# Kernel tuning notes

Measured on AMD Instinct MI355X. Metric: run time of the kernel, lower is better.

Reference implementation:

```python
import jax, jax.numpy as jnp
import numpy as np

BETA = 1.0
DEPTH = 10
LEVELS = DEPTH - 1          # decision levels along any root->leaf path
NUM_LEAVES = 2 ** LEVELS    # 512
NUM_INTERNAL = NUM_LEAVES - 1  # 511, heap-ordered: root=0, children 2i+1/2i+2


def _tree_paths():
    """For each leaf, the heap indices of its ancestors and the branch taken (0=left,1=right)."""
    anc = np.zeros((NUM_LEAVES, LEVELS), dtype=np.int32)
    bits = np.zeros((NUM_LEAVES, LEVELS), dtype=np.int32)
    for j in range(NUM_LEAVES):
        node = 0
        for t in range(LEVELS):
            bit = (j >> (LEVELS - 1 - t)) & 1
            anc[j, t] = node
            bits[j, t] = bit
            node = 2 * node + 1 + bit
    return jnp.asarray(anc), jnp.asarray(bits)

_ANC, _BITS = _tree_paths()


def setup_inputs() -> dict:
    key = jax.random.key(0)
    k1, k2, k3, k4 = jax.random.split(key, 4)
    B, F, K = 8192, 4096, 1000
    return {
        "xs": jax.random.normal(k1, (B, F), dtype=jnp.float32),
        "W": jax.random.normal(k2, (NUM_INTERNAL, F), dtype=jnp.float32) * (1.0 / np.sqrt(F)),
        "b": jax.random.normal(k3, (NUM_INTERNAL,), dtype=jnp.float32) * 0.01,
        "leaf_params": jax.random.normal(k4, (NUM_LEAVES, K), dtype=jnp.float32),
    }


def reference(xs, W, b, leaf_params):
    # All node projections as one GEMM: [B, NUM_INTERNAL]
    ps = jax.nn.sigmoid(BETA * (xs @ W.T + b))
    # Gather per-leaf ancestor probs: [B, NUM_LEAVES, LEVELS]
    g = ps[:, _ANC]
    edge = jnp.where(_BITS[None] == 1, g, 1.0 - g)
    leaf_prob = jnp.prod(edge, axis=-1)          # [B, NUM_LEAVES]
    dists = jax.nn.softmax(leaf_params, axis=-1)  # [NUM_LEAVES, K]
    return leaf_prob @ dists                      # [B, K]
```

## Files before the change

### kernel.cpp

```cpp
#include <hip/hip_runtime.h>


typedef __bf16 bf16x8 __attribute__((ext_vector_type(8)));
typedef float f32x4 __attribute__((ext_vector_type(4)));
typedef _Float16 f16x8 __attribute__((ext_vector_type(8)));

#define B_DIM 8192
#define F_DIM 4096
#define NI 511
#define NL 512
#define K_DIM 1000
#define KPAD 1024
#define SPLIT 2
#define KCHUNK 2048
#define NT_G1 32

#define W_BLKS  1024
#define SM_BLKS 512

__device__ inline unsigned short f2bf(float f) {
    unsigned int u = __float_as_uint(f);
    return (unsigned short)((u + 0x7FFFu + ((u >> 16) & 1u)) >> 16);
}
__device__ inline unsigned int pk_bf16(float a, float b) {
    return (unsigned int)f2bf(a) | ((unsigned int)f2bf(b) << 16);
}
__device__ inline unsigned int pk2_hu(float a, float b) {
    unsigned int ua = __float_as_uint(a) + 0x8000u;
    unsigned int ub = __float_as_uint(b) + 0x8000u;
    return __builtin_amdgcn_perm(ub, ua, 0x07060302u);
}

typedef __attribute__((address_space(1))) const unsigned int guint;
typedef __attribute__((address_space(3))) unsigned int luint;
__device__ inline void gload16(const unsigned short* g, unsigned short* l) {
    __builtin_amdgcn_global_load_lds((guint*)g, (luint*)l, 16, 0, 0);
}

__device__ inline bf16x8 ldb(const unsigned short* Lbase, int r, int kb) {
    const int g = (kb >> 3) ^ (r & 7);
    return *(const bf16x8*)&Lbase[r * 64 + g * 8];
}

__device__ inline float waveMax(float v) {
#pragma unroll
    for (int off = 32; off; off >>= 1) v = fmaxf(v, __shfl_down(v, off, 64));
    return v;
}
__device__ inline float waveSum(float v) {
#pragma unroll
    for (int off = 32; off; off >>= 1) v += __shfl_down(v, off, 64);
    return v;
}

__global__ __launch_bounds__(256) void prep_kernel(
    const float* __restrict__ W, unsigned short* __restrict__ Wb,
    const float* __restrict__ lp, unsigned short* __restrict__ dT)
{
    __shared__ float sred[8];
    const int bid = blockIdx.x;
    const int tid = threadIdx.x;

    if (bid < W_BLKS) {
        const size_t i = ((size_t)bid * 256 + tid) * 8;
        const int row = (int)(i >> 12);
        uint4 h = {0u, 0u, 0u, 0u};
        if (row < NI) {
            const float4 a = *(const float4*)(W + i);
            const float4 b = *(const float4*)(W + i + 4);
            h.x = pk_bf16(a.x, a.y);
            h.y = pk_bf16(a.z, a.w);
            h.z = pk_bf16(b.x, b.y);
            h.w = pk_bf16(b.z, b.w);
        }
        *(uint4*)(Wb + i) = h;
        return;
    }
    const int k = bid - W_BLKS;
    const int lane = tid & 63;
    const int wave = tid >> 6;
    const float* rowp = lp + (size_t)k * K_DIM;

    float vals[4];
    float mx = -3.0e38f;
#pragma unroll
    for (int c = 0; c < 4; ++c) {
        const int n = tid + c * 256;
        vals[c] = (n < K_DIM) ? rowp[n] : -3.0e38f;
        mx = fmaxf(mx, vals[c]);
    }
    mx = waveMax(mx);
    if (lane == 0) sred[wave] = mx;
    __syncthreads();
    const float gmax = fmaxf(fmaxf(sred[0], sred[1]), fmaxf(sred[2], sred[3]));

    float sum = 0.f;
#pragma unroll
    for (int c = 0; c < 4; ++c) {
        const int n = tid + c * 256;
        const float e = (n < K_DIM) ? __expf(vals[c] - gmax) : 0.f;
        vals[c] = e;
        sum += e;
    }
    sum = waveSum(sum);
    if (lane == 0) sred[4 + wave] = sum;
    __syncthreads();
    const float inv = 1.0f / (sred[4] + sred[5] + sred[6] + sred[7]);
#pragma unroll
    for (int c = 0; c < 4; ++c) {
        const int n = tid + c * 256;
        if (n < K_DIM) dT[(size_t)n * NL + k] = f2bf(vals[c] * inv);
    }
}

__global__ __launch_bounds__(256, 2) void gemm1_kernel(
    const float* __restrict__ A, const unsigned short* __restrict__ Bb,
    _Float16* __restrict__ part)
{
    __shared__ __align__(16) unsigned short Al[128 * 64];
    __shared__ __align__(16) unsigned short Bl[4][128 * 64];

    const int id = blockIdx.x;
    const int xcd = id & 7;
    const int j = id >> 3;
    const int nt = j & 3;
    const int z = (j >> 2) & 1;
    const int mhi = j >> 3;
    const int m0 = (mhi * 8 + xcd) * 128;
    const int n0 = nt * 128;
    const int kbeg = z * KCHUNK;

    const int tid = threadIdx.x;
    const int lane = tid & 63;
    const int wave = tid >> 6;
    const int wm = (wave >> 1) * 64;
    const int wn = (wave & 1) * 64;
    const int quad = lane >> 4;
    const int l16 = lane & 15;

    const int rowA = wave * 4 + (lane >> 4);
    const int q = lane & 15;
    const float* gA = A + (size_t)(m0 + rowA) * F_DIM + kbeg + q * 4;

    const int drb = lane >> 3;
    const int cb = ((lane & 7) ^ drb) * 8;
    const unsigned short* gB = Bb + (size_t)(n0 + wave * 8 + drb) * F_DIM + kbeg + cb;
    const int lBoff = wave * 8 * 64;

    const f32x4 zero = {0.f, 0.f, 0.f, 0.f};
    f32x4 acc[4][4];
#pragma unroll
    for (int i = 0; i < 4; ++i)
#pragma unroll
        for (int j2 = 0; j2 < 4; ++j2) acc[i][j2] = zero;

    f32x4 ab[2][8];
#pragma unroll
    for (int p = 0; p < 4; ++p)
        gload16(gB + (size_t)p * 32 * F_DIM, &Bl[0][lBoff + p * 2048]);
#pragma unroll
    for (int p = 0; p < 4; ++p)
        gload16(gB + 64 + (size_t)p * 32 * F_DIM, &Bl[1][lBoff + p * 2048]);
    __builtin_amdgcn_sched_barrier(0);
#pragma unroll
    for (int p = 0; p < 8; ++p)
        ab[0][p] = *(const f32x4*)(gA + (size_t)p * 16 * F_DIM);
#pragma unroll
    for (int p = 0; p < 8; ++p)
        ab[1][p] = *(const f32x4*)(gA + 64 + (size_t)p * 16 * F_DIM);
    __builtin_amdgcn_sched_barrier(0);

#define G1_ITER(T, DO_ISSUE, WCNT)                                             \
    {                                                                          \
        _Pragma("unroll") for (int p = 0; p < 8; ++p) {                        \
            const int r = rowA + p * 16;                                       \
            uint2 w;                                                           \
            w.x = pk2_hu(ab[(T) & 1][p].x, ab[(T) & 1][p].y);                  \
            w.y = pk2_hu(ab[(T) & 1][p].z, ab[(T) & 1][p].w);                  \
            *(uint2*)&Al[r * 64 + (((q >> 1) ^ (r & 7)) * 8) + (q & 1) * 4] = w;\
        }                                                                      \
        asm volatile("s_waitcnt vmcnt(" #WCNT ") lgkmcnt(0)" ::: "memory");    \
        __builtin_amdgcn_sched_barrier(0);                                     \
        __builtin_amdgcn_s_barrier();                                          \
        __builtin_amdgcn_sched_barrier(0);                                     \
        if (DO_ISSUE) {                                                        \
            _Pragma("unroll") for (int p = 0; p < 4; ++p)                      \
                gload16(gB + (size_t)((T) + 2) * 64 + (size_t)p * 32 * F_DIM,  \
                        &Bl[((T) + 2) & 3][lBoff + p * 2048]);                 \
            __builtin_amdgcn_sched_barrier(0);                                 \
            _Pragma("unroll") for (int p = 0; p < 8; ++p)                      \
                ab[(T) & 1][p] = *(const f32x4*)(gA + (size_t)((T) + 2) * 64   \
                                                 + (size_t)p * 16 * F_DIM);    \
        }                                                                      \
        _Pragma("unroll") for (int kk = 0; kk < 64; kk += 32) {                \
            const int kb = kk + quad * 8;                                      \
            bf16x8 av[4], bv[4];                                               \
            _Pragma("unroll") for (int i = 0; i < 4; ++i)                      \
                av[i] = ldb(Al, wm + i * 16 + l16, kb);                        \
            _Pragma("unroll") for (int j2 = 0; j2 < 4; ++j2)                   \
                bv[j2] = ldb(&Bl[(T) & 3][0], wn + j2 * 16 + l16, kb);         \
            _Pragma("unroll") for (int i = 0; i < 4; ++i)                      \
                _Pragma("unroll") for (int j2 = 0; j2 < 4; ++j2)               \
                    acc[i][j2] = __builtin_amdgcn_mfma_f32_16x16x32_bf16(      \
                        av[i], bv[j2], acc[i][j2], 0, 0, 0);                   \
        }                                                                      \
        __builtin_amdgcn_sched_barrier(0);                                     \
        __builtin_amdgcn_s_barrier();                                          \
        __builtin_amdgcn_sched_barrier(0);                                     \
    }

#pragma unroll 4
    for (int t = 0; t < NT_G1 - 4; ++t) G1_ITER(t, 1, 12);
    G1_ITER(28, 1, 12);
    G1_ITER(29, 1, 12);
    G1_ITER(30, 0, 12);
    G1_ITER(31, 0, 0);
#undef G1_ITER

    _Float16* dst = part + (size_t)z * ((size_t)B_DIM * NL);
#pragma unroll
    for (int i = 0; i < 4; ++i) {
        const int mbase = m0 + wm + i * 16 + quad * 4;
#pragma unroll
        for (int j2 = 0; j2 < 4; ++j2) {
            const int n = n0 + wn + j2 * 16 + l16;
#pragma unroll
            for (int r = 0; r < 4; ++r)
                dst[(size_t)(mbase + r) * NL + n] = (_Float16)acc[i][j2][r];
        }
    }
}

__global__ __launch_bounds__(256) void reduce_tree_kernel(
    const _Float16* __restrict__ part, const float* __restrict__ bvec,
    unsigned short* __restrict__ leafbf)
{
    __shared__ float bsh[NL];
    __shared__ float prow[4][NL];

    const int tid = threadIdx.x;
    bsh[tid] = (tid < NI) ? bvec[tid] : 0.0f;
    const int t2 = tid + 256;
    bsh[t2] = (t2 < NI) ? bvec[t2] : 0.0f;

    const int wave = tid >> 6;
    const int lane = tid & 63;
    const int row = blockIdx.x * 4 + wave;
    const size_t base = (size_t)row * NL + lane * 8;

    float v[8] = {0.f, 0.f, 0.f, 0.f, 0.f, 0.f, 0.f, 0.f};
#pragma unroll
    for (int s = 0; s < SPLIT; ++s) {
        const f16x8 h = *(const f16x8*)(part + (size_t)s * ((size_t)B_DIM * NL) + base);
#pragma unroll
        for (int e = 0; e < 8; ++e) v[e] += (float)h[e];
    }
    __syncthreads();

#pragma unroll
    for (int i = 0; i < 8; ++i) {
        const float x = v[i] + bsh[lane * 8 + i];
        prow[wave][lane * 8 + i] = 1.0f / (1.0f + __expf(-x));
    }
    __syncthreads();

    const float* pr = prow[wave];
    float pre = 1.0f;
    int pnode = 0;
#pragma unroll
    for (int t = 5; t >= 0; --t) {
        const int bit = (lane >> t) & 1;
        const float p = pr[pnode];
        pre *= bit ? p : (1.0f - p);
        pnode = 2 * pnode + 1 + bit;
    }
    unsigned short outs[8];
#pragma unroll
    for (int jj = 0; jj < 8; ++jj) {
        float prob = pre;
        int node = pnode;
#pragma unroll
        for (int t = 2; t >= 0; --t) {
            const int bit = (jj >> t) & 1;
            const float p = pr[node];
            prob *= bit ? p : (1.0f - p);
            node = 2 * node + 1 + bit;
        }
        outs[jj] = f2bf(prob);
    }
    uint4 r;
    r.x = (unsigned int)outs[0] | ((unsigned int)outs[1] << 16);
    r.y = (unsigned int)outs[2] | ((unsigned int)outs[3] << 16);
    r.z = (unsigned int)outs[4] | ((unsigned int)outs[5] << 16);
    r.w = (unsigned int)outs[6] | ((unsigned int)outs[7] << 16);
    *(uint4*)(leafbf + (size_t)row * NL + lane * 8) = r;
}

__global__ __launch_bounds__(256) void gemm2_kernel(
    const unsigned short* __restrict__ A, const unsigned short* __restrict__ Bm,
    float* __restrict__ out)
{
    __shared__ __align__(16) unsigned short Al[128 * 64];
    __shared__ __align__(16) unsigned short Bl[128 * 64];

    const int id = blockIdx.x;
    const int xcd = id & 7;
    const int j = id >> 3;
    const int nt = j & 7;
    const int mhi = j >> 3;
    const int m0 = (mhi * 8 + xcd) * 128;
    const int n0 = nt * 128;

    const int tid = threadIdx.x;
    const int lane = tid & 63;
    const int wave = tid >> 6;
    const int wm = (wave >> 1) * 64;
    const int wn = (wave & 1) * 64;
    const int quad = lane >> 4;
    const int l16 = lane & 15;

    const int drb = lane >> 3;
    const int cb = ((lane & 7) ^ drb) * 8;
    const unsigned short* gA = A + (size_t)(m0 + wave * 8 + drb) * NL + cb;
    const unsigned short* gB = Bm + (size_t)(n0 + wave * 8 + drb) * NL + cb;
    unsigned short* lA = &Al[wave * 8 * 64];
    unsigned short* lB = &Bl[wave * 8 * 64];

    const f32x4 zero = {0.f, 0.f, 0.f, 0.f};
    f32x4 acc[4][4];
#pragma unroll
    for (int i = 0; i < 4; ++i)
#pragma unroll
        for (int j2 = 0; j2 < 4; ++j2) acc[i][j2] = zero;

    for (int k0 = 0; k0 < NL; k0 += 64) {
#pragma unroll
        for (int p = 0; p < 4; ++p) {
            gload16(gA + k0 + (size_t)p * 32 * NL, lA + p * 2048);
            gload16(gB + k0 + (size_t)p * 32 * NL, lB + p * 2048);
        }
        __syncthreads();
#pragma unroll
        for (int kk = 0; kk < 64; kk += 32) {
            const int kb = kk + quad * 8;
            bf16x8 av[4], bv[4];
#pragma unroll
            for (int i = 0; i < 4; ++i)
                av[i] = ldb(Al, wm + i * 16 + l16, kb);
#pragma unroll
            for (int j2 = 0; j2 < 4; ++j2)
                bv[j2] = ldb(Bl, wn + j2 * 16 + l16, kb);
#pragma unroll
            for (int i = 0; i < 4; ++i)
#pragma unroll
                for (int j2 = 0; j2 < 4; ++j2)
                    acc[i][j2] = __builtin_amdgcn_mfma_f32_16x16x32_bf16(av[i], bv[j2], acc[i][j2], 0, 0, 0);
        }
        __syncthreads();
    }

#pragma unroll
    for (int i = 0; i < 4; ++i) {
        const int mbase = m0 + wm + i * 16 + quad * 4;
#pragma unroll
        for (int j2 = 0; j2 < 4; ++j2) {
            const int n = n0 + wn + j2 * 16 + l16;
            if (n < K_DIM) {
#pragma unroll
                for (int r = 0; r < 4; ++r)
                    out[(size_t)(mbase + r) * K_DIM + n] = acc[i][j2][r];
            }
        }
    }
}

extern "C" void kernel_launch(void* const* d_in, const int* in_sizes, int n_in,
                              void* d_out, int out_size, void* d_ws, size_t ws_size,
                              hipStream_t stream) {
    const float* xs = (const float*)d_in[0];
    const float* W  = (const float*)d_in[1];
    const float* b  = (const float*)d_in[2];
    const float* lp = (const float*)d_in[3];
    float* out = (float*)d_out;

    const size_t partB = (size_t)B_DIM * NL * 2;
    const size_t leafB = (size_t)B_DIM * NL * 2;
    const size_t dTB   = (size_t)KPAD * NL * 2;

    char* ws = (char*)d_ws;
    _Float16* part = (_Float16*)ws;
    unsigned short* leafbf = (unsigned short*)(ws + SPLIT * partB);
    unsigned short* dT = (unsigned short*)(ws + SPLIT * partB + leafB);
    unsigned short* Wb = (unsigned short*)(ws + SPLIT * partB + leafB + dTB);
    (void)ws_size;

    hipLaunchKernelGGL(prep_kernel, dim3(W_BLKS + SM_BLKS), dim3(256), 0, stream,
                       W, Wb, lp, dT);
    hipLaunchKernelGGL(gemm1_kernel, dim3(8 * 8 * 2 * 4), dim3(256), 0, stream,
                       xs, Wb, part);
    hipLaunchKernelGGL(reduce_tree_kernel, dim3(B_DIM / 4), dim3(256), 0, stream,
                       part, b, leafbf);
    hipLaunchKernelGGL(gemm2_kernel, dim3(8 * 8 * 8), dim3(256), 0, stream,
                       leafbf, dT, out);
}
```

Baseline: 263.7 us.

## Split gemm1 K three ways for higher occupancy; double-buffer gemm2 LDS loads

gemm1 now splits K into three chunks instead of two, so it launches 768 blocks instead of 512. To fit three blocks per CU it shrinks the B LDS ring from four stages to two. gemm2 gains a double-buffered LDS pipeline, so loads for the next K-slab overlap the MFMA work on the current one, replacing the old load-then-sync loop. This trades more fp16 partial-sum traffic and extra reduction work, plus a shallower prefetch in gemm1, for better occupancy and wave balance.

```diff
diff --git a/kernel.cpp b/kernel.cpp
--- a/kernel.cpp
+++ b/kernel.cpp
@@ -11,9 +11,7 @@
 #define NL 512
 #define K_DIM 1000
 #define KPAD 1024
-#define SPLIT 2
-#define KCHUNK 2048
-#define NT_G1 32
+#define SPLIT 3
 
 #define W_BLKS  1024
 #define SM_BLKS 512
@@ -113,22 +111,24 @@
     }
 }
 
-__global__ __launch_bounds__(256, 2) void gemm1_kernel(
+__global__ __launch_bounds__(256, 3) void gemm1_kernel(
     const float* __restrict__ A, const unsigned short* __restrict__ Bb,
     _Float16* __restrict__ part)
 {
     __shared__ __align__(16) unsigned short Al[128 * 64];
-    __shared__ __align__(16) unsigned short Bl[4][128 * 64];
+    __shared__ __align__(16) unsigned short Bl[2][128 * 64];
 
     const int id = blockIdx.x;
     const int xcd = id & 7;
     const int j = id >> 3;
     const int nt = j & 3;
-    const int z = (j >> 2) & 1;
-    const int mhi = j >> 3;
+    const int rem = j >> 2;
+    const int mhi = rem / 3;
+    const int z = rem - mhi * 3;
     const int m0 = (mhi * 8 + xcd) * 128;
     const int n0 = nt * 128;
-    const int kbeg = z * KCHUNK;
+    const int kbeg = z * 1408;
+    const int NT = (z == 2) ? 20 : 22;
 
     const int tid = threadIdx.x;
     const int lane = tid & 63;
@@ -158,9 +158,6 @@
 #pragma unroll
     for (int p = 0; p < 4; ++p)
         gload16(gB + (size_t)p * 32 * F_DIM, &Bl[0][lBoff + p * 2048]);
-#pragma unroll
-    for (int p = 0; p < 4; ++p)
-        gload16(gB + 64 + (size_t)p * 32 * F_DIM, &Bl[1][lBoff + p * 2048]);
     __builtin_amdgcn_sched_barrier(0);
 #pragma unroll
     for (int p = 0; p < 8; ++p)
@@ -170,27 +167,34 @@
         ab[1][p] = *(const f32x4*)(gA + 64 + (size_t)p * 16 * F_DIM);
     __builtin_amdgcn_sched_barrier(0);
 
-#define G1_ITER(T, DO_ISSUE, WCNT)                                             \
+#define G1_ITER(TVAL, PAR)                                                     \
     {                                                                          \
+        const int t_ = (TVAL);                                                 \
         _Pragma("unroll") for (int p = 0; p < 8; ++p) {                        \
             const int r = rowA + p * 16;                                       \
             uint2 w;                                                           \
-            w.x = pk2_hu(ab[(T) & 1][p].x, ab[(T) & 1][p].y);                  \
-            w.y = pk2_hu(ab[(T) & 1][p].z, ab[(T) & 1][p].w);                  \
+            w.x = pk2_hu(ab[PAR][p].x, ab[PAR][p].y);                          \
+            w.y = pk2_hu(ab[PAR][p].z, ab[PAR][p].w);                          \
             *(uint2*)&Al[r * 64 + (((q >> 1) ^ (r & 7)) * 8) + (q & 1) * 4] = w;\
         }                                                                      \
-        asm volatile("s_waitcnt vmcnt(" #WCNT ") lgkmcnt(0)" ::: "memory");    \
+        if (t_ < NT - 1) {                                                     \
+            asm volatile("s_waitcnt vmcnt(8) lgkmcnt(0)" ::: "memory");        \
+        } else {                                                               \
+            asm volatile("s_waitcnt vmcnt(0) lgkmcnt(0)" ::: "memory");        \
+        }                                                                      \
         __builtin_amdgcn_sched_barrier(0);                                     \
         __builtin_amdgcn_s_barrier();                                          \
         __builtin_amdgcn_sched_barrier(0);                                     \
-        if (DO_ISSUE) {                                                        \
+        if (t_ + 1 < NT) {                                                     \
             _Pragma("unroll") for (int p = 0; p < 4; ++p)                      \
-                gload16(gB + (size_t)((T) + 2) * 64 + (size_t)p * 32 * F_DIM,  \
-                        &Bl[((T) + 2) & 3][lBoff + p * 2048]);                 \
-            __builtin_amdgcn_sched_barrier(0);                                 \
+                gload16(gB + (size_t)(t_ + 1) * 64 + (size_t)p * 32 * F_DIM,   \
+                        &Bl[(PAR) ^ 1][lBoff + p * 2048]);                     \
+        }                                                                      \
+        __builtin_amdgcn_sched_barrier(0);                                     \
+        if (t_ + 2 < NT) {                                                     \
             _Pragma("unroll") for (int p = 0; p < 8; ++p)                      \
-                ab[(T) & 1][p] = *(const f32x4*)(gA + (size_t)((T) + 2) * 64   \
-                                                 + (size_t)p * 16 * F_DIM);    \
+                ab[PAR][p] = *(const f32x4*)(gA + (size_t)(t_ + 2) * 64        \
+                                             + (size_t)p * 16 * F_DIM);       \
         }                                                                      \
         _Pragma("unroll") for (int kk = 0; kk < 64; kk += 32) {                \
             const int kb = kk + quad * 8;                                      \
@@ -198,7 +202,7 @@
             _Pragma("unroll") for (int i = 0; i < 4; ++i)                      \
                 av[i] = ldb(Al, wm + i * 16 + l16, kb);                        \
             _Pragma("unroll") for (int j2 = 0; j2 < 4; ++j2)                   \
-                bv[j2] = ldb(&Bl[(T) & 3][0], wn + j2 * 16 + l16, kb);         \
+                bv[j2] = ldb(&Bl[PAR][0], wn + j2 * 16 + l16, kb);             \
             _Pragma("unroll") for (int i = 0; i < 4; ++i)                      \
                 _Pragma("unroll") for (int j2 = 0; j2 < 4; ++j2)               \
                     acc[i][j2] = __builtin_amdgcn_mfma_f32_16x16x32_bf16(      \
@@ -209,12 +213,10 @@
         __builtin_amdgcn_sched_barrier(0);                                     \
     }
 
-#pragma unroll 4
-    for (int t = 0; t < NT_G1 - 4; ++t) G1_ITER(t, 1, 12);
-    G1_ITER(28, 1, 12);
-    G1_ITER(29, 1, 12);
-    G1_ITER(30, 0, 12);
-    G1_ITER(31, 0, 0);
+    for (int th = 0; th < NT / 2; ++th) {
+        G1_ITER(2 * th, 0);
+        G1_ITER(2 * th + 1, 1);
+    }
 #undef G1_ITER
 
     _Float16* dst = part + (size_t)z * ((size_t)B_DIM * NL);
@@ -296,12 +298,12 @@
     *(uint4*)(leafbf + (size_t)row * NL + lane * 8) = r;
 }
 
-__global__ __launch_bounds__(256) void gemm2_kernel(
+__global__ __launch_bounds__(256, 2) void gemm2_kernel(
     const unsigned short* __restrict__ A, const unsigned short* __restrict__ Bm,
     float* __restrict__ out)
 {
-    __shared__ __align__(16) unsigned short Al[128 * 64];
-    __shared__ __align__(16) unsigned short Bl[128 * 64];
+    __shared__ __align__(16) unsigned short Al[2][128 * 64];
+    __shared__ __align__(16) unsigned short Bl[2][128 * 64];
 
     const int id = blockIdx.x;
     const int xcd = id & 7;
@@ -323,8 +325,7 @@
     const int cb = ((lane & 7) ^ drb) * 8;
     const unsigned short* gA = A + (size_t)(m0 + wave * 8 + drb) * NL + cb;
     const unsigned short* gB = Bm + (size_t)(n0 + wave * 8 + drb) * NL + cb;
-    unsigned short* lA = &Al[wave * 8 * 64];
-    unsigned short* lB = &Bl[wave * 8 * 64];
+    const int loff = wave * 8 * 64;
 
     const f32x4 zero = {0.f, 0.f, 0.f, 0.f};
     f32x4 acc[4][4];
@@ -333,30 +334,51 @@
 #pragma unroll
         for (int j2 = 0; j2 < 4; ++j2) acc[i][j2] = zero;
 
-    for (int k0 = 0; k0 < NL; k0 += 64) {
-#pragma unroll
-        for (int p = 0; p < 4; ++p) {
-            gload16(gA + k0 + (size_t)p * 32 * NL, lA + p * 2048);
-            gload16(gB + k0 + (size_t)p * 32 * NL, lB + p * 2048);
-        }
-        __syncthreads();
+#pragma unroll
+    for (int p = 0; p < 4; ++p) {
+        gload16(gA + (size_t)p * 32 * NL, &Al[0][loff + p * 2048]);
+        gload16(gB + (size_t)p * 32 * NL, &Bl[0][loff + p * 2048]);
+    }
+    __builtin_amdgcn_sched_barrier(0);
+
+#pragma unroll
+    for (int t = 0; t < 8; ++t) {
+        if (t + 1 < 8) {
+#pragma unroll
+            for (int p = 0; p < 4; ++p) {
+                gload16(gA + (size_t)(t + 1) * 64 + (size_t)p * 32 * NL,
+                        &Al[(t + 1) & 1][loff + p * 2048]);
+                gload16(gB + (size_t)(t + 1) * 64 + (size_t)p * 32 * NL,
+                        &Bl[(t + 1) & 1][loff + p * 2048]);
+            }
+            __builtin_amdgcn_sched_barrier(0);
+            asm volatile("s_waitcnt vmcnt(8)" ::: "memory");
+        } else {
+            __builtin_amdgcn_sched_barrier(0);
+            asm volatile("s_waitcnt vmcnt(0)" ::: "memory");
+        }
+        __builtin_amdgcn_sched_barrier(0);
+        __builtin_amdgcn_s_barrier();
+        __builtin_amdgcn_sched_barrier(0);
 #pragma unroll
         for (int kk = 0; kk < 64; kk += 32) {
             const int kb = kk + quad * 8;
             bf16x8 av[4], bv[4];
 #pragma unroll
             for (int i = 0; i < 4; ++i)
-                av[i] = ldb(Al, wm + i * 16 + l16, kb);
+                av[i] = ldb(&Al[t & 1][0], wm + i * 16 + l16, kb);
 #pragma unroll
             for (int j2 = 0; j2 < 4; ++j2)
-                bv[j2] = ldb(Bl, wn + j2 * 16 + l16, kb);
+                bv[j2] = ldb(&Bl[t & 1][0], wn + j2 * 16 + l16, kb);
 #pragma unroll
             for (int i = 0; i < 4; ++i)
 #pragma unroll
                 for (int j2 = 0; j2 < 4; ++j2)
                     acc[i][j2] = __builtin_amdgcn_mfma_f32_16x16x32_bf16(av[i], bv[j2], acc[i][j2], 0, 0, 0);
         }
-        __syncthreads();
+        __builtin_amdgcn_sched_barrier(0);
+        __builtin_amdgcn_s_barrier();
+        __builtin_amdgcn_sched_barrier(0);
     }
 
 #pragma unroll
@@ -396,7 +418,7 @@
 
     hipLaunchKernelGGL(prep_kernel, dim3(W_BLKS + SM_BLKS), dim3(256), 0, stream,
                        W, Wb, lp, dT);
-    hipLaunchKernelGGL(gemm1_kernel, dim3(8 * 8 * 2 * 4), dim3(256), 0, stream,
+    hipLaunchKernelGGL(gemm1_kernel, dim3(768), dim3(256), 0, stream,
                        xs, Wb, part);
     hipLaunchKernelGGL(reduce_tree_kernel, dim3(B_DIM / 4), dim3(256), 0, stream,
                        part, b, leafbf);
```

After: 312.0 us. 18.3% more time.
